# Kernel tuning notes

Hardware: AMD Instinct MI355X
Metric: run time of the kernel (lower is better)

Reference implementation:

```python
import jax, jax.numpy as jnp
import numpy as np

N = 50000      # nodes
E = 800000     # edges
CIN = 128
CH = 128
COUT = 64
EPS = 1e-5     # BatchNorm eps


def setup_inputs() -> dict:
    key = jax.random.key(0)
    ks = jax.random.split(key, 16)
    s = 0.1  # weight scale for numerical stability
    return {
        "x": jax.random.normal(ks[0], (N, CIN), jnp.float32),
        "edge_index": jax.random.randint(ks[1], (2, E), 0, N, jnp.int32),
        "edge_weights": jax.random.uniform(ks[2], (E,), jnp.float32),
        "w1": jax.random.normal(ks[3], (CIN, CH), jnp.float32) * s,
        "b1": jnp.zeros((CH,), jnp.float32),
        "bn1_g": jnp.ones((CH,), jnp.float32),
        "bn1_b": jnp.zeros((CH,), jnp.float32),
        "bn1_m": jax.random.normal(ks[4], (CH,), jnp.float32) * 0.1,
        "bn1_v": jax.random.uniform(ks[5], (CH,), jnp.float32) + 0.5,
        "conv_ws": jax.random.normal(ks[6], (2, CH, CH), jnp.float32) * s,
        "conv_bs": jnp.zeros((2, CH), jnp.float32),
        "bns_g": jnp.ones((2, CH), jnp.float32),
        "bns_b": jnp.zeros((2, CH), jnp.float32),
        "bns_m": jax.random.normal(ks[7], (2, CH), jnp.float32) * 0.1,
        "bns_v": jax.random.uniform(ks[8], (2, CH), jnp.float32) + 0.5,
        "lin1_w": jax.random.normal(ks[9], (CH, CH), jnp.float32) * s,
        "lin1_b": jnp.zeros((CH,), jnp.float32),
        "lin2_w": jax.random.normal(ks[10], (CH, COUT), jnp.float32) * s,
        "lin2_b": jnp.zeros((COUT,), jnp.float32),
    }


def _bn(h, g, b, m, v):
    # BatchNorm1d in eval mode: running statistics
    return (h - m) * jax.lax.rsqrt(v + EPS) * g + b


def _gcn(h, w, b, src, dst, norm, n):
    # GCNConv: out[dst] += norm_e * (h @ W)[src]  (self loops already in src/dst)
    h = h @ w
    msg = h[src] * norm[:, None]                 # [E+N, CH]
    return jax.ops.segment_sum(msg, dst, num_segments=n) + b


def reference(x, edge_index, edge_weights, w1, b1, bn1_g, bn1_b, bn1_m, bn1_v,
              conv_ws, conv_bs, bns_g, bns_b, bns_m, bns_v,
              lin1_w, lin1_b, lin2_w, lin2_b):
    n = x.shape[0]
    loop = jnp.arange(n, dtype=edge_index.dtype)
    src = jnp.concatenate([edge_index[0], loop])
    dst = jnp.concatenate([edge_index[1], loop])
    ew = jnp.concatenate([edge_weights, jnp.ones((n,), edge_weights.dtype)])
    # symmetric degree normalization (PyG gcn_norm)
    deg = jax.ops.segment_sum(ew, dst, num_segments=n)
    dis = jnp.where(deg > 0, jax.lax.rsqrt(deg), 0.0)
    norm = dis[src] * ew * dis[dst]

    lrelu = jax.nn.leaky_relu  # slope 0.01, matches F.leaky_relu default
    h = lrelu(_bn(_gcn(x, w1, b1, src, dst, norm, n), bn1_g, bn1_b, bn1_m, bn1_v))
    for i in range(conv_ws.shape[0]):
        h = lrelu(_bn(_gcn(h, conv_ws[i], conv_bs[i], src, dst, norm, n),
                      bns_g[i], bns_b[i], bns_m[i], bns_v[i]) + h)
    h = lrelu(h @ lin1_w + lin1_b)
    # dropout is identity in eval mode
    return h @ lin2_w + lin2_b
```

## Files before the change

kernel.cpp:

```cpp
#include <hip/hip_runtime.h>
#include <hip/hip_bf16.h>


constexpr int   NN    = 50000;
constexpr int   EE    = 800000;
constexpr int   CH    = 128;
constexpr int   SLOTS = 64;
constexpr int   NBUK  = 782;
constexpr int   RCAP  = 2048;
constexpr int   EPB   = 2048;
constexpr float EPS   = 1e-5f;

typedef __attribute__((ext_vector_type(8))) short bf16x8;
typedef __attribute__((ext_vector_type(4))) float f32x4;
typedef unsigned long long u64;
typedef unsigned short u16;

__device__ inline u16 f2bf_rne(float f) {
  unsigned u = __float_as_uint(f);
  unsigned r = u + 0x7fffu + ((u >> 16) & 1u);
  return (u16)(r >> 16);
}
__device__ inline float bf2f(unsigned h16) {
  return __uint_as_float(h16 << 16);
}


__global__ __launch_bounds__(256) void bin_kernel(const int* __restrict__ ei,
                                                  const float* __restrict__ ew,
                                                  unsigned* __restrict__ gcur,
                                                  u64* __restrict__ bins) {
  __shared__ unsigned cnt[NBUK];
  __shared__ unsigned base[NBUK];
  const int tid = threadIdx.x;
  for (int b = tid; b < NBUK; b += 256) cnt[b] = 0;
  __syncthreads();
  const int e0 = blockIdx.x * EPB;
  unsigned pk[8]; u16 bkt[8]; u16 rnk[8]; unsigned char dl[8];
  #pragma unroll
  for (int i = 0; i < 8; i++) {
    int e = e0 + i * 256 + tid;
    if (e < EE) {
      int s = ei[e], d = ei[EE + e];
      float w = ew[e];
      bkt[i] = (u16)(d >> 6);
      dl[i]  = (unsigned char)(d & 63);
      pk[i]  = ((unsigned)f2bf_rne(w) << 16) | (unsigned)s;
      rnk[i] = (u16)atomicAdd(&cnt[bkt[i]], 1u);
    } else bkt[i] = 0xffffu;
  }
  __syncthreads();
  for (int b = tid; b < NBUK; b += 256) {
    unsigned c = cnt[b];
    base[b] = c ? atomicAdd(&gcur[b * 16], c) : 0u;
  }
  __syncthreads();
  #pragma unroll
  for (int i = 0; i < 8; i++) {
    if (bkt[i] == 0xffffu) continue;
    unsigned pos = base[bkt[i]] + rnk[i];
    if (pos < RCAP)
      bins[(size_t)bkt[i] * RCAP + pos] = ((u64)dl[i] << 32) | pk[i];
  }
}


__global__ __launch_bounds__(256) void scatter_kernel(const unsigned* __restrict__ gcur,
                                                      const u64* __restrict__ bins,
                                                      unsigned* __restrict__ ell,
                                                      float* __restrict__ dis) {
  __shared__ unsigned rank[64];
  __shared__ float    wsum[64];
  const int b   = blockIdx.x;
  const int tid = threadIdx.x;
  if (tid < 64) { rank[tid] = 1u; wsum[tid] = 0.f; }
  __syncthreads();
  unsigned cnt = gcur[b * 16];
  if (cnt > RCAP) cnt = RCAP;
  const u64* src = bins + (size_t)b * RCAP;
  for (unsigned i = tid; i < cnt; i += 256) {
    u64 v = src[i];
    unsigned pk = (unsigned)v;
    unsigned dl = (unsigned)(v >> 32);
    unsigned r = atomicAdd(&rank[dl], 1u);
    if (r < SLOTS)
      ell[((size_t)(b * 64 + dl)) * SLOTS + r] = pk;
    atomicAdd(&wsum[dl], bf2f(pk >> 16));
  }
  __syncthreads();
  if (tid < 64) {
    int node = b * 64 + tid;
    if (node < NN) {
      unsigned c = rank[tid];
      if (c > SLOTS) c = SLOTS;
      ell[(size_t)node * SLOTS] = c;
      dis[node] = rsqrtf(1.0f + wsum[tid]);
    }
  }
}

constexpr int NB_WZ = (73728 + 384 + 255) / 256;

__global__ void wswz_kernel(
    const float* __restrict__ w1, const float* __restrict__ bn1_g, const float* __restrict__ bn1_v,
    const float* __restrict__ conv_ws, const float* __restrict__ bns_g, const float* __restrict__ bns_v,
    const float* __restrict__ lin1_w, const float* __restrict__ lin2_w,
    const float* __restrict__ b1, const float* __restrict__ bn1_b, const float* __restrict__ bn1_m,
    const float* __restrict__ conv_bs, const float* __restrict__ bns_b, const float* __restrict__ bns_m,
    u16* __restrict__ w1h, u16* __restrict__ w1l,
    u16* __restrict__ c0h, u16* __restrict__ c0l,
    u16* __restrict__ c1h, u16* __restrict__ c1l,
    u16* __restrict__ l1h, u16* __restrict__ l1l,
    u16* __restrict__ l2h, u16* __restrict__ l2l,
    float* __restrict__ beff)
{
  int idx = blockIdx.x * 256 + threadIdx.x;
  if (idx >= 73728) {
    int r = idx - 73728;
    if (r >= 384) return;
    int l = r >> 7, c = r & 127;
    float bc, gg, bb, mm, vv;
    if (l == 0) { bc = b1[c]; gg = bn1_g[c]; bb = bn1_b[c]; mm = bn1_m[c]; vv = bn1_v[c]; }
    else {
      int o = (l - 1) * 128 + c;
      bc = conv_bs[o]; gg = bns_g[o]; bb = bns_b[o]; mm = bns_m[o]; vv = bns_v[o];
    }
    beff[r] = (bc - mm) * gg * rsqrtf(vv + EPS) + bb;
    return;
  }
  const float* W; const float* g = nullptr; const float* v = nullptr;
  u16 *hi, *lo; int CO = 128; int local;
  if      (idx < 16384) { W = w1;              g = bn1_g;     v = bn1_v;     hi = w1h; lo = w1l; local = idx; }
  else if (idx < 32768) { W = conv_ws;         g = bns_g;     v = bns_v;     hi = c0h; lo = c0l; local = idx - 16384; }
  else if (idx < 49152) { W = conv_ws + 16384; g = bns_g+128; v = bns_v+128; hi = c1h; lo = c1l; local = idx - 32768; }
  else if (idx < 65536) { W = lin1_w;                                        hi = l1h; lo = l1l; local = idx - 49152; }
  else                  { W = lin2_w;                                        hi = l2h; lo = l2l; local = idx - 65536; CO = 64; }
  int k = local / CO, n = local % CO;
  float w = W[local];
  if (g) w *= g[n] * rsqrtf(v[n] + EPS);
  int NCT = CO / 16;
  int kchunk = k >> 5, kin = k & 31, quad = kin >> 3, j = kin & 7;
  int ct = n >> 4, l = (quad << 4) | (n & 15);
  size_t pos = ((size_t)(kchunk * NCT + ct) * 64 + l) * 8 + j;
  u16 h = f2bf_rne(w);
  hi[pos] = h;
  lo[pos] = f2bf_rne(w - bf2f(h));
}

__global__ __launch_bounds__(256) void gemm1_kernel(
    const float* __restrict__ Ain,
    const u16* __restrict__ Whi, const u16* __restrict__ Wlo,
    const float* __restrict__ dis, u16* __restrict__ Cout)
{
  __shared__ float lds[64][CH + 4];
  const int tid  = threadIdx.x;
  const int wave = tid >> 6;
  const int lane = tid & 63;
  const int quad = lane >> 4;
  const int mrow = lane & 15;
  const int row0 = blockIdx.x * 64;

  int arow = row0 + wave * 16 + mrow;
  if (arow >= NN) arow = NN - 1;

  bf16x8 ahi[4], alo[4];
  const float* Ar = Ain + (size_t)arow * CH;
  #pragma unroll
  for (int c = 0; c < 4; c++) {
    int off = c * 32 + quad * 8;
    float4 f0 = *(const float4*)(Ar + off);
    float4 f1 = *(const float4*)(Ar + off + 4);
    float f[8] = {f0.x, f0.y, f0.z, f0.w, f1.x, f1.y, f1.z, f1.w};
    #pragma unroll
    for (int j = 0; j < 8; j++) {
      u16 h = f2bf_rne(f[j]);
      ahi[c][j] = (short)h;
      alo[c][j] = (short)f2bf_rne(f[j] - bf2f(h));
    }
  }

  f32x4 acc[8];
  #pragma unroll
  for (int t = 0; t < 8; t++) acc[t] = (f32x4){0.f, 0.f, 0.f, 0.f};
  #pragma unroll
  for (int c = 0; c < 4; c++) {
    #pragma unroll
    for (int t = 0; t < 8; t++) {
      size_t base = ((size_t)(c * 8 + t) * 64 + lane) * 8;
      bf16x8 bh = *(const bf16x8*)(Whi + base);
      bf16x8 bl = *(const bf16x8*)(Wlo + base);
      acc[t] = __builtin_amdgcn_mfma_f32_16x16x32_bf16(ahi[c], bh, acc[t], 0, 0, 0);
      acc[t] = __builtin_amdgcn_mfma_f32_16x16x32_bf16(alo[c], bh, acc[t], 0, 0, 0);
      acc[t] = __builtin_amdgcn_mfma_f32_16x16x32_bf16(ahi[c], bl, acc[t], 0, 0, 0);
    }
  }

  #pragma unroll
  for (int t = 0; t < 8; t++)
    #pragma unroll
    for (int r = 0; r < 4; r++)
      lds[wave * 16 + quad * 4 + r][t * 16 + mrow] = acc[t][r];
  __syncthreads();

  #pragma unroll
  for (int i = tid; i < 64 * CH / 4; i += 256) {
    int row = (i * 4) / CH;
    int col = (i * 4) % CH;
    int grow = row0 + row;
    if (grow >= NN) continue;
    float rs = dis[grow];
    const float* lp = &lds[row][col];
    u16* cp = (u16*)Cout + (size_t)grow * CH + col;
    unsigned p0 = ((unsigned)f2bf_rne(lp[1] * rs) << 16) | f2bf_rne(lp[0] * rs);
    unsigned p1 = ((unsigned)f2bf_rne(lp[3] * rs) << 16) | f2bf_rne(lp[2] * rs);
    *(uint2*)cp = make_uint2(p0, p1);
  }
}

template<bool RES, bool WH>
__device__ __forceinline__ void gather4_grp(
    const u16* __restrict__ hwin, const unsigned* __restrict__ ell,
    const float* __restrict__ dis, const float* __restrict__ beff,
    const u16* __restrict__ res, u16* __restrict__ hout,
    unsigned* __restrict__ hsbase,
    int nbase, int lane, int sub, int grp)
{
  const int node = nbase + grp;
  const size_t ebase = (size_t)node * SLOTS + sub;
  unsigned w0 = ell[ebase];
  unsigned w1 = ell[ebase + 16];
  unsigned w2 = ell[ebase + 32];
  unsigned w3 = ell[ebase + 48];

  int cme = __shfl((int)w0, grp << 4); if (cme > SLOTS) cme = SLOTS;
  int c0 = __shfl((int)w0, 0),  c1 = __shfl((int)w0, 16);
  int c2 = __shfl((int)w0, 32), c3 = __shfl((int)w0, 48);
  int cmax = max(max(c0, c1), max(c2, c3)); if (cmax > SLOTS) cmax = SLOTS;

  float a[8] = {0.f, 0.f, 0.f, 0.f, 0.f, 0.f, 0.f, 0.f};
  const u16* hrow = hwin + sub * 8;

  for (int j = 0; j < cmax; j += 8) {
    uint4 hQ[8]; float wQ[8];
    #pragma unroll
    for (int u = 0; u < 8; u++) {
      int jj = j + u;
      int k = jj >> 4;
      unsigned wsel = k == 0 ? w0 : (k == 1 ? w1 : (k == 2 ? w2 : w3));
      unsigned e = (unsigned)__shfl((int)wsel, (grp << 4) | (jj & 15));
      float wv = (jj == 0) ? 1.0f : bf2f(e >> 16);
      unsigned s = (jj == 0) ? (unsigned)node : (e & 0xffffu);
      if (jj >= cme) { wv = 0.f; s = (unsigned)node; }
      wQ[u] = wv;
      hQ[u] = *(const uint4*)(hrow + (size_t)s * CH);
    }
    #pragma unroll
    for (int u = 0; u < 8; u++) {
      float w = wQ[u];
      a[0] = fmaf(w, bf2f(hQ[u].x & 0xffffu), a[0]); a[1] = fmaf(w, bf2f(hQ[u].x >> 16), a[1]);
      a[2] = fmaf(w, bf2f(hQ[u].y & 0xffffu), a[2]); a[3] = fmaf(w, bf2f(hQ[u].y >> 16), a[3]);
      a[4] = fmaf(w, bf2f(hQ[u].z & 0xffffu), a[4]); a[5] = fmaf(w, bf2f(hQ[u].z >> 16), a[5]);
      a[6] = fmaf(w, bf2f(hQ[u].w & 0xffffu), a[6]); a[7] = fmaf(w, bf2f(hQ[u].w >> 16), a[7]);
    }
  }

  float disd = dis[node];
  int c = sub * 8;
  float4 be0 = *(const float4*)(beff + c);
  float4 be1 = *(const float4*)(beff + c + 4);
  float y[8];
  y[0] = a[0] * disd + be0.x; y[1] = a[1] * disd + be0.y;
  y[2] = a[2] * disd + be0.z; y[3] = a[3] * disd + be0.w;
  y[4] = a[4] * disd + be1.x; y[5] = a[5] * disd + be1.y;
  y[6] = a[6] * disd + be1.z; y[7] = a[7] * disd + be1.w;
  if constexpr (RES) {
    uint4 rr = *(const uint4*)(res + (size_t)node * CH + c);
    y[0] += bf2f(rr.x & 0xffffu); y[1] += bf2f(rr.x >> 16);
    y[2] += bf2f(rr.y & 0xffffu); y[3] += bf2f(rr.y >> 16);
    y[4] += bf2f(rr.z & 0xffffu); y[5] += bf2f(rr.z >> 16);
    y[6] += bf2f(rr.w & 0xffffu); y[7] += bf2f(rr.w >> 16);
  }
  #pragma unroll
  for (int k = 0; k < 8; k++) y[k] = y[k] > 0.f ? y[k] : 0.01f * y[k];
  uint4 o;
  o.x = ((unsigned)f2bf_rne(y[1]) << 16) | f2bf_rne(y[0]);
  o.y = ((unsigned)f2bf_rne(y[3]) << 16) | f2bf_rne(y[2]);
  o.z = ((unsigned)f2bf_rne(y[5]) << 16) | f2bf_rne(y[4]);
  o.w = ((unsigned)f2bf_rne(y[7]) << 16) | f2bf_rne(y[6]);
  if constexpr (WH)
    *(uint4*)(hout + (size_t)node * CH + c) = o;
  *(uint4*)&hsbase[grp * 68 + sub * 4] = o;
}

template<bool RES>
__global__ __launch_bounds__(256, 6) void fuse_kernel(
    const u16* __restrict__ hwin,
    const unsigned* __restrict__ ell, const float* __restrict__ dis,
    const float* __restrict__ beff, const u16* __restrict__ res,
    const u16* __restrict__ Whi, const u16* __restrict__ Wlo,
    u16* __restrict__ hout, u16* __restrict__ hwout)
{
  __shared__ unsigned hs[16][68];
  const int tid  = threadIdx.x;
  const int wave = tid >> 6;
  const int lane = tid & 63;
  const int sub  = lane & 15;
  const int grp  = lane >> 4;
  const int row0 = blockIdx.x * 16;

  gather4_grp<RES, true>(hwin, ell, dis, beff, res, hout,
                         &hs[wave * 4][0], row0 + wave * 4, lane, sub, grp);
  __syncthreads();

  bf16x8 af[4];
  #pragma unroll
  for (int c = 0; c < 4; c++)
    af[c] = *(const bf16x8*)&hs[sub][c * 16 + grp * 4];

  f32x4 acc[2];
  #pragma unroll
  for (int t = 0; t < 2; t++) acc[t] = (f32x4){0.f, 0.f, 0.f, 0.f};
  #pragma unroll
  for (int c = 0; c < 4; c++) {
    #pragma unroll
    for (int t = 0; t < 2; t++) {
      size_t base = ((size_t)(c * 8 + wave * 2 + t) * 64 + lane) * 8;
      bf16x8 bh = *(const bf16x8*)(Whi + base);
      bf16x8 bl = *(const bf16x8*)(Wlo + base);
      acc[t] = __builtin_amdgcn_mfma_f32_16x16x32_bf16(af[c], bh, acc[t], 0, 0, 0);
      acc[t] = __builtin_amdgcn_mfma_f32_16x16x32_bf16(af[c], bl, acc[t], 0, 0, 0);
    }
  }

  #pragma unroll
  for (int r = 0; r < 4; r++) {
    int grow = row0 + grp * 4 + r;
    if (grow >= NN) continue;
    float rs = dis[grow];
    #pragma unroll
    for (int t = 0; t < 2; t++)
      hwout[(size_t)grow * CH + wave * 32 + t * 16 + sub] = f2bf_rne(acc[t][r] * rs);
  }
}

__global__ __launch_bounds__(256, 6) void fuse_last_kernel(
    const u16* __restrict__ hwin,
    const unsigned* __restrict__ ell, const float* __restrict__ dis,
    const float* __restrict__ beff, const u16* __restrict__ res,
    const u16* __restrict__ l1h, const u16* __restrict__ l1l,
    const float* __restrict__ b1,
    const u16* __restrict__ l2h, const u16* __restrict__ l2l,
    const float* __restrict__ b2, float* __restrict__ out)
{
  __shared__ unsigned hs[16][68];
  __shared__ float    fs[16][132];
  const int tid  = threadIdx.x;
  const int wave = tid >> 6;
  const int lane = tid & 63;
  const int sub  = lane & 15;
  const int grp  = lane >> 4;
  const int row0 = blockIdx.x * 16;

  gather4_grp<true, false>(hwin, ell, dis, beff, res, nullptr,
                           &hs[wave * 4][0], row0 + wave * 4, lane, sub, grp);
  __syncthreads();

  bf16x8 af[4];
  #pragma unroll
  for (int c = 0; c < 4; c++)
    af[c] = *(const bf16x8*)&hs[sub][c * 16 + grp * 4];

  f32x4 acc[2];
  #pragma unroll
  for (int t = 0; t < 2; t++) acc[t] = (f32x4){0.f, 0.f, 0.f, 0.f};
  #pragma unroll
  for (int c = 0; c < 4; c++) {
    #pragma unroll
    for (int t = 0; t < 2; t++) {
      size_t base = ((size_t)(c * 8 + wave * 2 + t) * 64 + lane) * 8;
      bf16x8 bh = *(const bf16x8*)(l1h + base);
      bf16x8 bl = *(const bf16x8*)(l1l + base);
      acc[t] = __builtin_amdgcn_mfma_f32_16x16x32_bf16(af[c], bh, acc[t], 0, 0, 0);
      acc[t] = __builtin_amdgcn_mfma_f32_16x16x32_bf16(af[c], bl, acc[t], 0, 0, 0);
    }
  }
  #pragma unroll
  for (int t = 0; t < 2; t++) {
    int col = wave * 32 + t * 16 + sub;
    float bb = b1[col];
    #pragma unroll
    for (int r = 0; r < 4; r++) {
      float x = acc[t][r] + bb;
      x = x > 0.f ? x : 0.01f * x;
      fs[grp * 4 + r][col] = x;
    }
  }
  __syncthreads();

  f32x4 acc2 = (f32x4){0.f, 0.f, 0.f, 0.f};
  #pragma unroll
  for (int c = 0; c < 4; c++) {
    bf16x8 ahi, alo;
    const float* lp = &fs[sub][c * 32 + grp * 8];
    float4 f0 = *(const float4*)lp;
    float4 f1 = *(const float4*)(lp + 4);
    float f[8] = {f0.x, f0.y, f0.z, f0.w, f1.x, f1.y, f1.z, f1.w};
    #pragma unroll
    for (int j = 0; j < 8; j++) {
      u16 h = f2bf_rne(f[j]);
      ahi[j] = (short)h;
      alo[j] = (short)f2bf_rne(f[j] - bf2f(h));
    }
    size_t base = ((size_t)(c * 4 + wave) * 64 + lane) * 8;
    bf16x8 bh = *(const bf16x8*)(l2h + base);
    bf16x8 bl = *(const bf16x8*)(l2l + base);
    acc2 = __builtin_amdgcn_mfma_f32_16x16x32_bf16(ahi, bh, acc2, 0, 0, 0);
    acc2 = __builtin_amdgcn_mfma_f32_16x16x32_bf16(alo, bh, acc2, 0, 0, 0);
    acc2 = __builtin_amdgcn_mfma_f32_16x16x32_bf16(ahi, bl, acc2, 0, 0, 0);
  }
  {
    float bb = b2[wave * 16 + sub];
    #pragma unroll
    for (int r = 0; r < 4; r++) {
      int grow = row0 + grp * 4 + r;
      if (grow < NN)
        out[(size_t)grow * 64 + wave * 16 + sub] = acc2[r] + bb;
    }
  }
}


extern "C" void kernel_launch(void* const* d_in, const int* in_sizes, int n_in,
                              void* d_out, int out_size, void* d_ws, size_t ws_size,
                              hipStream_t stream) {
  const float* x       = (const float*)d_in[0];
  const int*   ei      = (const int*)  d_in[1];
  const float* ew      = (const float*)d_in[2];
  const float* w1      = (const float*)d_in[3];
  const float* b1      = (const float*)d_in[4];
  const float* bn1_g   = (const float*)d_in[5];
  const float* bn1_b   = (const float*)d_in[6];
  const float* bn1_m   = (const float*)d_in[7];
  const float* bn1_v   = (const float*)d_in[8];
  const float* conv_ws = (const float*)d_in[9];
  const float* conv_bs = (const float*)d_in[10];
  const float* bns_g   = (const float*)d_in[11];
  const float* bns_b   = (const float*)d_in[12];
  const float* bns_m   = (const float*)d_in[13];
  const float* bns_v   = (const float*)d_in[14];
  const float* lin1_w  = (const float*)d_in[15];
  const float* lin1_b  = (const float*)d_in[16];
  const float* lin2_w  = (const float*)d_in[17];
  const float* lin2_b  = (const float*)d_in[18];
  float* out = (float*)d_out;

  size_t off = 0;
  auto alloc = [&](size_t elems) -> void* {
    void* p = (char*)d_ws + off * 4;
    off += (elems + 3) & ~(size_t)3;
    return p;
  };
  unsigned* gcur = (unsigned*)alloc(NBUK * 16);
  u64*      bins = (u64*)     alloc((size_t)NBUK * RCAP * 2);
  unsigned* ell  = (unsigned*)alloc((size_t)NN * SLOTS);
  float*    dis  = (float*)   alloc(NN);
  float*    beff = (float*)   alloc(3 * CH);
  u16*      hwa  = (u16*)     alloc((size_t)NN * CH / 2);
  u16*      hwb  = (u16*)     alloc((size_t)NN * CH / 2);
  u16*      h1   = (u16*)     alloc((size_t)NN * CH / 2);
  u16*      h2   = (u16*)     alloc((size_t)NN * CH / 2);
  u16* w1h = (u16*)alloc(CH * CH / 2); u16* w1l = (u16*)alloc(CH * CH / 2);
  u16* c0h = (u16*)alloc(CH * CH / 2); u16* c0l = (u16*)alloc(CH * CH / 2);
  u16* c1h = (u16*)alloc(CH * CH / 2); u16* c1l = (u16*)alloc(CH * CH / 2);
  u16* l1h = (u16*)alloc(CH * CH / 2); u16* l1l = (u16*)alloc(CH * CH / 2);
  u16* l2h = (u16*)alloc(CH * 64 / 2); u16* l2l = (u16*)alloc(CH * 64 / 2);

  const int nb_bin  = (EE + EPB - 1) / EPB;
  const int nb_gemm = (NN + 63) / 64;
  const int nb_fuse = (NN + 15) / 16;
  dim3 B(256);

  hipMemsetAsync(gcur, 0, NBUK * 16 * sizeof(unsigned), stream);
  bin_kernel    <<<nb_bin, B, 0, stream>>>(ei, ew, gcur, bins);
  scatter_kernel<<<NBUK,   B, 0, stream>>>(gcur, bins, ell, dis);

  wswz_kernel<<<NB_WZ, B, 0, stream>>>(w1, bn1_g, bn1_v, conv_ws, bns_g, bns_v,
      lin1_w, lin2_w, b1, bn1_b, bn1_m, conv_bs, bns_b, bns_m,
      w1h, w1l, c0h, c0l, c1h, c1l, l1h, l1l, l2h, l2l, beff);

  gemm1_kernel<<<nb_gemm, B, 0, stream>>>(x, w1h, w1l, dis, hwa);

  fuse_kernel<false><<<nb_fuse, B, 0, stream>>>(hwa, ell, dis, beff, nullptr,
      c0h, c0l, h1, hwb);

  fuse_kernel<true><<<nb_fuse, B, 0, stream>>>(hwb, ell, dis, beff + CH, h1,
      c1h, c1l, h2, hwa);

  fuse_last_kernel<<<nb_fuse, B, 0, stream>>>(hwa, ell, dis, beff + 2 * CH, h2,
      l1h, l1l, lin1_b, l2h, l2l, lin2_b, out);
}
```

Baseline: 333.7 us.

## Build ELL with direct global atomics and gather with wave-wide edge split

Replaces the two-pass bucket binning (block-local counts, then per-bucket scatter) with one kernel that does a global atomicAdd per edge into per-node rank and weight-sum arrays, plus a small finalize kernel. The gather now processes one node at a time per wave, splitting its edges across the four 16-lane groups and reducing with shuffles, which balances work when degrees differ. The fuse kernel's hw output is staged through LDS so global stores are coalesced. Global atomics on random destinations may contend more than the binned approach, and the extra syncthreads add some latency.

```diff
diff --git a/kernel.cpp b/kernel.cpp
--- a/kernel.cpp
+++ b/kernel.cpp
@@ -6,9 +6,6 @@
 constexpr int   EE    = 800000;
 constexpr int   CH    = 128;
 constexpr int   SLOTS = 64;
-constexpr int   NBUK  = 782;
-constexpr int   RCAP  = 2048;
-constexpr int   EPB   = 2048;
 constexpr float EPS   = 1e-5f;
 
 typedef __attribute__((ext_vector_type(8))) short bf16x8;
@@ -26,77 +23,32 @@
 }
 
 
-__global__ __launch_bounds__(256) void bin_kernel(const int* __restrict__ ei,
-                                                  const float* __restrict__ ew,
-                                                  unsigned* __restrict__ gcur,
-                                                  u64* __restrict__ bins) {
-  __shared__ unsigned cnt[NBUK];
-  __shared__ unsigned base[NBUK];
-  const int tid = threadIdx.x;
-  for (int b = tid; b < NBUK; b += 256) cnt[b] = 0;
-  __syncthreads();
-  const int e0 = blockIdx.x * EPB;
-  unsigned pk[8]; u16 bkt[8]; u16 rnk[8]; unsigned char dl[8];
-  #pragma unroll
-  for (int i = 0; i < 8; i++) {
-    int e = e0 + i * 256 + tid;
-    if (e < EE) {
-      int s = ei[e], d = ei[EE + e];
-      float w = ew[e];
-      bkt[i] = (u16)(d >> 6);
-      dl[i]  = (unsigned char)(d & 63);
-      pk[i]  = ((unsigned)f2bf_rne(w) << 16) | (unsigned)s;
-      rnk[i] = (u16)atomicAdd(&cnt[bkt[i]], 1u);
-    } else bkt[i] = 0xffffu;
-  }
-  __syncthreads();
-  for (int b = tid; b < NBUK; b += 256) {
-    unsigned c = cnt[b];
-    base[b] = c ? atomicAdd(&gcur[b * 16], c) : 0u;
-  }
-  __syncthreads();
-  #pragma unroll
-  for (int i = 0; i < 8; i++) {
-    if (bkt[i] == 0xffffu) continue;
-    unsigned pos = base[bkt[i]] + rnk[i];
-    if (pos < RCAP)
-      bins[(size_t)bkt[i] * RCAP + pos] = ((u64)dl[i] << 32) | pk[i];
-  }
-}
-
-
-__global__ __launch_bounds__(256) void scatter_kernel(const unsigned* __restrict__ gcur,
-                                                      const u64* __restrict__ bins,
-                                                      unsigned* __restrict__ ell,
-                                                      float* __restrict__ dis) {
-  __shared__ unsigned rank[64];
-  __shared__ float    wsum[64];
-  const int b   = blockIdx.x;
-  const int tid = threadIdx.x;
-  if (tid < 64) { rank[tid] = 1u; wsum[tid] = 0.f; }
-  __syncthreads();
-  unsigned cnt = gcur[b * 16];
-  if (cnt > RCAP) cnt = RCAP;
-  const u64* src = bins + (size_t)b * RCAP;
-  for (unsigned i = tid; i < cnt; i += 256) {
-    u64 v = src[i];
-    unsigned pk = (unsigned)v;
-    unsigned dl = (unsigned)(v >> 32);
-    unsigned r = atomicAdd(&rank[dl], 1u);
-    if (r < SLOTS)
-      ell[((size_t)(b * 64 + dl)) * SLOTS + r] = pk;
-    atomicAdd(&wsum[dl], bf2f(pk >> 16));
-  }
-  __syncthreads();
-  if (tid < 64) {
-    int node = b * 64 + tid;
-    if (node < NN) {
-      unsigned c = rank[tid];
-      if (c > SLOTS) c = SLOTS;
-      ell[(size_t)node * SLOTS] = c;
-      dis[node] = rsqrtf(1.0f + wsum[tid]);
-    }
-  }
+__global__ __launch_bounds__(256) void ellb_kernel(const int* __restrict__ ei,
+                                                   const float* __restrict__ ew,
+                                                   unsigned* __restrict__ rank,
+                                                   float* __restrict__ wsum,
+                                                   unsigned* __restrict__ ell) {
+  int e = blockIdx.x * 256 + threadIdx.x;
+  if (e >= EE) return;
+  int s = ei[e], d = ei[EE + e];
+  u16 wb = f2bf_rne(ew[e]);
+  unsigned pk = ((unsigned)wb << 16) | (unsigned)s;
+  unsigned r = atomicAdd(&rank[d], 1u);
+  if (r < SLOTS - 1)
+    ell[(size_t)d * SLOTS + 1 + r] = pk;
+  atomicAdd(&wsum[d], bf2f(wb));
+}
+
+__global__ __launch_bounds__(256) void ellf_kernel(const unsigned* __restrict__ rank,
+                                                   const float* __restrict__ wsum,
+                                                   unsigned* __restrict__ ell,
+                                                   float* __restrict__ dis) {
+  int n = blockIdx.x * 256 + threadIdx.x;
+  if (n >= NN) return;
+  unsigned c = rank[n] + 1;
+  if (c > SLOTS) c = SLOTS;
+  ell[(size_t)n * SLOTS] = c;
+  dis[n] = rsqrtf(1.0f + wsum[n]);
 }
 
 constexpr int NB_WZ = (73728 + 384 + 255) / 256;
@@ -218,78 +170,85 @@
 }
 
 template<bool RES, bool WH>
-__device__ __forceinline__ void gather4_grp(
+__device__ __forceinline__ void gather4_qw(
     const u16* __restrict__ hwin, const unsigned* __restrict__ ell,
     const float* __restrict__ dis, const float* __restrict__ beff,
     const u16* __restrict__ res, u16* __restrict__ hout,
     unsigned* __restrict__ hsbase,
     int nbase, int lane, int sub, int grp)
 {
-  const int node = nbase + grp;
-  const size_t ebase = (size_t)node * SLOTS + sub;
-  unsigned w0 = ell[ebase];
-  unsigned w1 = ell[ebase + 16];
-  unsigned w2 = ell[ebase + 32];
-  unsigned w3 = ell[ebase + 48];
-
-  int cme = __shfl((int)w0, grp << 4); if (cme > SLOTS) cme = SLOTS;
-  int c0 = __shfl((int)w0, 0),  c1 = __shfl((int)w0, 16);
-  int c2 = __shfl((int)w0, 32), c3 = __shfl((int)w0, 48);
-  int cmax = max(max(c0, c1), max(c2, c3)); if (cmax > SLOTS) cmax = SLOTS;
-
-  float a[8] = {0.f, 0.f, 0.f, 0.f, 0.f, 0.f, 0.f, 0.f};
-  const u16* hrow = hwin + sub * 8;
-
-  for (int j = 0; j < cmax; j += 8) {
-    uint4 hQ[8]; float wQ[8];
-    #pragma unroll
-    for (int u = 0; u < 8; u++) {
-      int jj = j + u;
-      int k = jj >> 4;
-      unsigned wsel = k == 0 ? w0 : (k == 1 ? w1 : (k == 2 ? w2 : w3));
-      unsigned e = (unsigned)__shfl((int)wsel, (grp << 4) | (jj & 15));
-      float wv = (jj == 0) ? 1.0f : bf2f(e >> 16);
-      unsigned s = (jj == 0) ? (unsigned)node : (e & 0xffffu);
-      if (jj >= cme) { wv = 0.f; s = (unsigned)node; }
-      wQ[u] = wv;
-      hQ[u] = *(const uint4*)(hrow + (size_t)s * CH);
-    }
-    #pragma unroll
-    for (int u = 0; u < 8; u++) {
-      float w = wQ[u];
-      a[0] = fmaf(w, bf2f(hQ[u].x & 0xffffu), a[0]); a[1] = fmaf(w, bf2f(hQ[u].x >> 16), a[1]);
-      a[2] = fmaf(w, bf2f(hQ[u].y & 0xffffu), a[2]); a[3] = fmaf(w, bf2f(hQ[u].y >> 16), a[3]);
-      a[4] = fmaf(w, bf2f(hQ[u].z & 0xffffu), a[4]); a[5] = fmaf(w, bf2f(hQ[u].z >> 16), a[5]);
-      a[6] = fmaf(w, bf2f(hQ[u].w & 0xffffu), a[6]); a[7] = fmaf(w, bf2f(hQ[u].w >> 16), a[7]);
-    }
-  }
-
-  float disd = dis[node];
-  int c = sub * 8;
-  float4 be0 = *(const float4*)(beff + c);
-  float4 be1 = *(const float4*)(beff + c + 4);
-  float y[8];
-  y[0] = a[0] * disd + be0.x; y[1] = a[1] * disd + be0.y;
-  y[2] = a[2] * disd + be0.z; y[3] = a[3] * disd + be0.w;
-  y[4] = a[4] * disd + be1.x; y[5] = a[5] * disd + be1.y;
-  y[6] = a[6] * disd + be1.z; y[7] = a[7] * disd + be1.w;
-  if constexpr (RES) {
-    uint4 rr = *(const uint4*)(res + (size_t)node * CH + c);
-    y[0] += bf2f(rr.x & 0xffffu); y[1] += bf2f(rr.x >> 16);
-    y[2] += bf2f(rr.y & 0xffffu); y[3] += bf2f(rr.y >> 16);
-    y[4] += bf2f(rr.z & 0xffffu); y[5] += bf2f(rr.z >> 16);
-    y[6] += bf2f(rr.w & 0xffffu); y[7] += bf2f(rr.w >> 16);
-  }
-  #pragma unroll
-  for (int k = 0; k < 8; k++) y[k] = y[k] > 0.f ? y[k] : 0.01f * y[k];
-  uint4 o;
-  o.x = ((unsigned)f2bf_rne(y[1]) << 16) | f2bf_rne(y[0]);
-  o.y = ((unsigned)f2bf_rne(y[3]) << 16) | f2bf_rne(y[2]);
-  o.z = ((unsigned)f2bf_rne(y[5]) << 16) | f2bf_rne(y[4]);
-  o.w = ((unsigned)f2bf_rne(y[7]) << 16) | f2bf_rne(y[6]);
-  if constexpr (WH)
-    *(uint4*)(hout + (size_t)node * CH + c) = o;
-  *(uint4*)&hsbase[grp * 68 + sub * 4] = o;
+  int nd0 = nbase < NN ? nbase : NN - 1;
+  unsigned wcur = ell[(size_t)nd0 * SLOTS + lane];
+  for (int r = 0; r < 4; r++) {
+    int node = nbase + r;
+    int nd = node < NN ? node : NN - 1;
+    unsigned myword = wcur;
+    if (r < 3) {
+      int n2 = node + 1 < NN ? node + 1 : NN - 1;
+      wcur = ell[(size_t)n2 * SLOTS + lane];
+    }
+    int cnt = __shfl((int)myword, 0);
+    if (cnt > SLOTS) cnt = SLOTS;
+    float a[8] = {0.f, 0.f, 0.f, 0.f, 0.f, 0.f, 0.f, 0.f};
+    for (int j = 0; j < cnt; j += 16) {
+      unsigned sidx[4]; float wv[4];
+      #pragma unroll
+      for (int q = 0; q < 4; q++) {
+        int jj = j + q * 4 + grp;
+        unsigned e = (unsigned)__shfl((int)myword, jj & 63);
+        float    w = (jj == 0) ? 1.0f : bf2f(e >> 16);
+        unsigned s = (jj == 0) ? (unsigned)nd : (e & 0xffffu);
+        if (jj >= cnt) { w = 0.f; s = (unsigned)nd; }
+        sidx[q] = s; wv[q] = w;
+      }
+      uint4 h[4];
+      #pragma unroll
+      for (int q = 0; q < 4; q++)
+        h[q] = *(const uint4*)(hwin + (size_t)sidx[q] * CH + sub * 8);
+      #pragma unroll
+      for (int q = 0; q < 4; q++) {
+        float w = wv[q];
+        a[0] = fmaf(w, bf2f(h[q].x & 0xffffu), a[0]); a[1] = fmaf(w, bf2f(h[q].x >> 16), a[1]);
+        a[2] = fmaf(w, bf2f(h[q].y & 0xffffu), a[2]); a[3] = fmaf(w, bf2f(h[q].y >> 16), a[3]);
+        a[4] = fmaf(w, bf2f(h[q].z & 0xffffu), a[4]); a[5] = fmaf(w, bf2f(h[q].z >> 16), a[5]);
+        a[6] = fmaf(w, bf2f(h[q].w & 0xffffu), a[6]); a[7] = fmaf(w, bf2f(h[q].w >> 16), a[7]);
+      }
+    }
+    #pragma unroll
+    for (int k = 0; k < 8; k++) {
+      a[k] += __shfl_xor(a[k], 16);
+      a[k] += __shfl_xor(a[k], 32);
+    }
+    if (grp == 0) {
+      float disd = dis[nd];
+      int c = sub * 8;
+      float4 be0 = *(const float4*)(beff + c);
+      float4 be1 = *(const float4*)(beff + c + 4);
+      float y[8];
+      y[0] = a[0] * disd + be0.x; y[1] = a[1] * disd + be0.y;
+      y[2] = a[2] * disd + be0.z; y[3] = a[3] * disd + be0.w;
+      y[4] = a[4] * disd + be1.x; y[5] = a[5] * disd + be1.y;
+      y[6] = a[6] * disd + be1.z; y[7] = a[7] * disd + be1.w;
+      if constexpr (RES) {
+        uint4 rr = *(const uint4*)(res + (size_t)nd * CH + c);
+        y[0] += bf2f(rr.x & 0xffffu); y[1] += bf2f(rr.x >> 16);
+        y[2] += bf2f(rr.y & 0xffffu); y[3] += bf2f(rr.y >> 16);
+        y[4] += bf2f(rr.z & 0xffffu); y[5] += bf2f(rr.z >> 16);
+        y[6] += bf2f(rr.w & 0xffffu); y[7] += bf2f(rr.w >> 16);
+      }
+      #pragma unroll
+      for (int k = 0; k < 8; k++) y[k] = y[k] > 0.f ? y[k] : 0.01f * y[k];
+      uint4 o;
+      o.x = ((unsigned)f2bf_rne(y[1]) << 16) | f2bf_rne(y[0]);
+      o.y = ((unsigned)f2bf_rne(y[3]) << 16) | f2bf_rne(y[2]);
+      o.z = ((unsigned)f2bf_rne(y[5]) << 16) | f2bf_rne(y[4]);
+      o.w = ((unsigned)f2bf_rne(y[7]) << 16) | f2bf_rne(y[6]);
+      if constexpr (WH) {
+        if (node < NN) *(uint4*)(hout + (size_t)node * CH + c) = o;
+      }
+      *(uint4*)&hsbase[r * 68 + sub * 4] = o;
+    }
+  }
 }
 
 template<bool RES>
@@ -308,14 +267,15 @@
   const int grp  = lane >> 4;
   const int row0 = blockIdx.x * 16;
 
-  gather4_grp<RES, true>(hwin, ell, dis, beff, res, hout,
-                         &hs[wave * 4][0], row0 + wave * 4, lane, sub, grp);
+  gather4_qw<RES, true>(hwin, ell, dis, beff, res, hout,
+                        &hs[wave * 4][0], row0 + wave * 4, lane, sub, grp);
   __syncthreads();
 
   bf16x8 af[4];
   #pragma unroll
   for (int c = 0; c < 4; c++)
     af[c] = *(const bf16x8*)&hs[sub][c * 16 + grp * 4];
+  __syncthreads();
 
   f32x4 acc[2];
   #pragma unroll
@@ -332,14 +292,21 @@
     }
   }
 
+  u16* hs16 = (u16*)&hs[0][0];
   #pragma unroll
   for (int r = 0; r < 4; r++) {
-    int grow = row0 + grp * 4 + r;
-    if (grow >= NN) continue;
-    float rs = dis[grow];
+    int row = grp * 4 + r;
+    float rs = dis[row0 + row];
     #pragma unroll
     for (int t = 0; t < 2; t++)
-      hwout[(size_t)grow * CH + wave * 32 + t * 16 + sub] = f2bf_rne(acc[t][r] * rs);
+      hs16[row * 136 + wave * 32 + t * 16 + sub] = f2bf_rne(acc[t][r] * rs);
+  }
+  __syncthreads();
+  {
+    int row   = tid >> 4;
+    int chunk = tid & 15;
+    uint4 o = *(const uint4*)(hs16 + row * 136 + chunk * 8);
+    *(uint4*)(hwout + (size_t)(row0 + row) * CH + chunk * 8) = o;
   }
 }
 
@@ -361,8 +328,8 @@
   const int grp  = lane >> 4;
   const int row0 = blockIdx.x * 16;
 
-  gather4_grp<true, false>(hwin, ell, dis, beff, res, nullptr,
-                           &hs[wave * 4][0], row0 + wave * 4, lane, sub, grp);
+  gather4_qw<true, false>(hwin, ell, dis, beff, res, nullptr,
+                          &hs[wave * 4][0], row0 + wave * 4, lane, sub, grp);
   __syncthreads();
 
   bf16x8 af[4];
@@ -460,9 +427,9 @@
     off += (elems + 3) & ~(size_t)3;
     return p;
   };
-  unsigned* gcur = (unsigned*)alloc(NBUK * 16);
-  u64*      bins = (u64*)     alloc((size_t)NBUK * RCAP * 2);
   unsigned* ell  = (unsigned*)alloc((size_t)NN * SLOTS);
+  unsigned* rank = (unsigned*)alloc(NN);
+  float*    wsum = (float*)   alloc(NN);
   float*    dis  = (float*)   alloc(NN);
   float*    beff = (float*)   alloc(3 * CH);
   u16*      hwa  = (u16*)     alloc((size_t)NN * CH / 2);
@@ -475,14 +442,16 @@
   u16* l1h = (u16*)alloc(CH * CH / 2); u16* l1l = (u16*)alloc(CH * CH / 2);
   u16* l2h = (u16*)alloc(CH * 64 / 2); u16* l2l = (u16*)alloc(CH * 64 / 2);
 
-  const int nb_bin  = (EE + EPB - 1) / EPB;
+  const int nb_ell  = (EE + 255) / 256;
+  const int nb_node = (NN + 255) / 256;
   const int nb_gemm = (NN + 63) / 64;
   const int nb_fuse = (NN + 15) / 16;
   dim3 B(256);
 
-  hipMemsetAsync(gcur, 0, NBUK * 16 * sizeof(unsigned), stream);
-  bin_kernel    <<<nb_bin, B, 0, stream>>>(ei, ew, gcur, bins);
-  scatter_kernel<<<NBUK,   B, 0, stream>>>(gcur, bins, ell, dis);
+  hipMemsetAsync(rank, 0, NN * sizeof(unsigned), stream);
+  hipMemsetAsync(wsum, 0, NN * sizeof(float), stream);
+  ellb_kernel<<<nb_ell,  B, 0, stream>>>(ei, ew, rank, wsum, ell);
+  ellf_kernel<<<nb_node, B, 0, stream>>>(rank, wsum, ell, dis);
 
   wswz_kernel<<<NB_WZ, B, 0, stream>>>(w1, bn1_g, bn1_v, conv_ws, bns_g, bns_v,
       lin1_w, lin2_w, b1, bn1_b, bn1_m, conv_bs, bns_b, bns_m,
```

Result: slower. 355.5 us (+6.5%).
